# Kernel tuning notes

Hardware: AMD Instinct MI355X
Metric: run time of the kernel (lower is better)

Reference implementation:

```python
import jax, jax.numpy as jnp
import numpy as np

B, T, D = 16, 2048, 64


def setup_inputs() -> dict:
    key = jax.random.key(0)
    kq, kk, kv, kb = jax.random.split(key, 4)
    q = jax.random.normal(kq, (B, T, D), dtype=jnp.float32)
    k = jax.random.normal(kk, (B, T, D), dtype=jnp.float32)
    v = jax.random.normal(kv, (B, T, D), dtype=jnp.float32)
    add_attn = jax.random.normal(kb, (B, T, T), dtype=jnp.float32)
    return {"q": q, "k": k, "v": v, "add_attn": add_attn}


def reference(q, k, v, add_attn):
    # scale = 1/sqrt(head_dim), the standard value passed by callers
    scale = 1.0 / jnp.sqrt(jnp.asarray(q.shape[-1], dtype=q.dtype))
    # [B, T, T] attention logits: bmm(q, k^T) * scale + additive bias
    attn = jnp.einsum('btd,bsd->bts', q, k) * scale + add_attn
    # softmax over keys (dim=2); dropout p=0.0 is identity
    attn = jax.nn.softmax(attn, axis=2)
    # [B, T, D] weighted values
    output = jnp.einsum('bts,bsd->btd', attn, v)
    return (output, attn)
```

## Files before the change

kernel.cpp:

```cpp
#include <hip/hip_runtime.h>
#include <stdint.h>

#define NB 16
#define NT 2048
#define ND 64

typedef __attribute__((ext_vector_type(8))) short bf16x8;
typedef __attribute__((ext_vector_type(4))) float f32x4;
typedef __attribute__((ext_vector_type(4))) _Float16 f16x4;

__device__ __forceinline__ unsigned short f2bf(float f) {
    union { float f; unsigned u; } v; v.f = f;
    unsigned r = v.u + 0x7fffu + ((v.u >> 16) & 1u);
    return (unsigned short)(r >> 16);
}
__device__ __forceinline__ unsigned short f2h(float f) {
    union { _Float16 h; unsigned short u; } v; v.h = (_Float16)f; return v.u;
}

__global__ __launch_bounds__(256) void prep_k(const float* __restrict__ Q,
                                              const float* __restrict__ K,
                                              const float* __restrict__ V,
                                              unsigned short* __restrict__ qbf,
                                              unsigned short* __restrict__ kbf,
                                              unsigned short* __restrict__ vt)
{
    const size_t i = (size_t)blockIdx.x * 256 + threadIdx.x;
    const int which = blockIdx.y;
    if (which == 2) {
        float4 v4 = ((const float4*)V)[i];
        const int d4 = (int)(i & 15);
        const int t  = (int)((i >> 4) & (NT - 1));
        const int b  = (int)(i >> 15);
        unsigned short* base = vt + ((size_t)b * ND + d4 * 4) * NT + t;
        base[0]      = f2h(v4.x);
        base[NT]     = f2h(v4.y);
        base[2 * NT] = f2h(v4.z);
        base[3 * NT] = f2h(v4.w);
    } else {
        const float4* src = (which == 0) ? (const float4*)Q : (const float4*)K;
        unsigned short* dst = (which == 0) ? qbf : kbf;
        float4 v4 = src[i];
        union { unsigned short s[4]; unsigned long long ll; } u;
        u.s[0] = f2bf(v4.x); u.s[1] = f2bf(v4.y);
        u.s[2] = f2bf(v4.z); u.s[3] = f2bf(v4.w);
        *(unsigned long long*)(dst + 4 * i) = u.ll;
    }
}

__global__ __launch_bounds__(512, 4)
void attn_onepass(const unsigned short* __restrict__ qbf,
                  const unsigned short* __restrict__ kbf,
                  const unsigned short* __restrict__ vt,
                  const float* __restrict__ Bias,
                  float* __restrict__ Out,
                  float* __restrict__ Attn)
{
    const int flat = blockIdx.x + (NT / 16) * blockIdx.y;
    const int lin  = (flat & 7) * 256 + (flat >> 3);
    const int b    = lin >> 7;
    const int q0   = (lin & 127) * 16;

    const int tid = threadIdx.x, w = tid >> 6, lane = tid & 63;
    const int n = lane & 15, qd = lane >> 4;
    const int kw0 = w * 256;

    __shared__ float s_rs[8][16];
    __shared__ float s_o[8 * 16 * 68];

    const unsigned short* qp = qbf + ((size_t)(b * NT + q0 + n)) * ND + qd * 8;
    const bf16x8 qf0 = *(const bf16x8*)qp;
    const bf16x8 qf1 = *(const bf16x8*)(qp + 32);
    const float* Bb = Bias + ((size_t)b * NT + q0 + n) * NT;
    float* Ab = Attn + ((size_t)b * NT + q0 + n) * NT;
    const unsigned short* vtb = vt + (size_t)b * ND * NT + (size_t)n * NT;
    const unsigned short* kbp = kbf + ((size_t)(b * NT + kw0 + n)) * ND + qd * 8;
    const float* bbp = Bb + kw0 + qd * 4;

    f16x4 ev[16];
    bf16x8 kb0[2], kb1[2];
    float4 bb[4];
#pragma unroll
    for (int i = 0; i < 2; ++i) {
        const unsigned short* kp = kbp + (size_t)(16 * i) * ND;
        kb0[i] = *(const bf16x8*)kp;
        kb1[i] = *(const bf16x8*)(kp + 32);
    }
#pragma unroll
    for (int i = 0; i < 4; ++i)
        bb[i] = *(const float4*)(bbp + 16 * i);
    __builtin_amdgcn_sched_barrier(0);

    float rs = 0.f;
#pragma unroll
    for (int t = 0; t < 16; ++t) {
        const bf16x8 kf0 = kb0[t & 1];
        const bf16x8 kf1 = kb1[t & 1];
        const float4 bs = bb[t & 3];
        f32x4 acc = {0.f, 0.f, 0.f, 0.f};
        acc = __builtin_amdgcn_mfma_f32_16x16x32_bf16(kf0, qf0, acc, 0, 0, 0);
        acc = __builtin_amdgcn_mfma_f32_16x16x32_bf16(kf1, qf1, acc, 0, 0, 0);
        float e0 = __expf(__builtin_fmaf(acc[0], 0.125f, bs.x - 2.0f));
        float e1 = __expf(__builtin_fmaf(acc[1], 0.125f, bs.y - 2.0f));
        float e2 = __expf(__builtin_fmaf(acc[2], 0.125f, bs.z - 2.0f));
        float e3 = __expf(__builtin_fmaf(acc[3], 0.125f, bs.w - 2.0f));
        union { _Float16 h[4]; f16x4 v; } u;
        u.h[0] = (_Float16)e0; u.h[1] = (_Float16)e1;
        u.h[2] = (_Float16)e2; u.h[3] = (_Float16)e3;
        ev[t] = u.v;
        rs += (e0 + e1) + (e2 + e3);
        __builtin_amdgcn_sched_barrier(0);
        if (t + 2 < 16) {
            const unsigned short* kp = kbp + (size_t)(16 * (t + 2)) * ND;
            kb0[t & 1] = *(const bf16x8*)kp;
            kb1[t & 1] = *(const bf16x8*)(kp + 32);
        }
        if (t + 4 < 16)
            bb[t & 3] = *(const float4*)(bbp + 16 * (t + 4));
        __builtin_amdgcn_sched_barrier(0);
    }

    f16x4 vr0[2][4], vr1[2][4];
#pragma unroll
    for (int i = 0; i < 2; ++i)
#pragma unroll
        for (int dt = 0; dt < 4; ++dt) {
            const unsigned short* vp = vtb + kw0 + 32 * i + qd * 4 + (size_t)dt * 16 * NT;
            vr0[i][dt] = *(const f16x4*)(const void*)vp;
            vr1[i][dt] = *(const f16x4*)(const void*)(vp + 16);
        }
    __builtin_amdgcn_sched_barrier(0);

    rs += __shfl_xor(rs, 16, 64);
    rs += __shfl_xor(rs, 32, 64);
    if (lane < 16) s_rs[w][lane] = rs;
    __syncthreads();
    const float tot = ((s_rs[0][n] + s_rs[1][n]) + (s_rs[2][n] + s_rs[3][n])) +
                      ((s_rs[4][n] + s_rs[5][n]) + (s_rs[6][n] + s_rs[7][n]));
    const float inv = 1.0f / tot;

    f32x4 oacc[4];
#pragma unroll
    for (int dt = 0; dt < 4; ++dt) oacc[dt] = (f32x4){0.f, 0.f, 0.f, 0.f};

#pragma unroll
    for (int tp = 0; tp < 8; ++tp) {
        const int key0 = kw0 + 32 * tp;
        const f16x4 e0v = ev[2 * tp];
        const f16x4 e1v = ev[2 * tp + 1];
        float4 s0, s1;
        s0.x = (float)e0v[0] * inv; s0.y = (float)e0v[1] * inv;
        s0.z = (float)e0v[2] * inv; s0.w = (float)e0v[3] * inv;
        s1.x = (float)e1v[0] * inv; s1.y = (float)e1v[1] * inv;
        s1.z = (float)e1v[2] * inv; s1.w = (float)e1v[3] * inv;
        *(float4*)(Ab + key0 + qd * 4) = s0;
        *(float4*)(Ab + key0 + 16 + qd * 4) = s1;
#pragma unroll
        for (int dt = 0; dt < 4; ++dt) {
            oacc[dt] = __builtin_amdgcn_mfma_f32_16x16x16f16(vr0[tp & 1][dt], e0v, oacc[dt], 0, 0, 0);
            oacc[dt] = __builtin_amdgcn_mfma_f32_16x16x16f16(vr1[tp & 1][dt], e1v, oacc[dt], 0, 0, 0);
        }
        __builtin_amdgcn_sched_barrier(0);
        if (tp + 2 < 8) {
#pragma unroll
            for (int dt = 0; dt < 4; ++dt) {
                const unsigned short* vp =
                    vtb + kw0 + 32 * (tp + 2) + qd * 4 + (size_t)dt * 16 * NT;
                vr0[tp & 1][dt] = *(const f16x4*)(const void*)vp;
                vr1[tp & 1][dt] = *(const f16x4*)(const void*)(vp + 16);
            }
        }
        __builtin_amdgcn_sched_barrier(0);
    }

#pragma unroll
    for (int dt = 0; dt < 4; ++dt) {
        float4 t4;
        t4.x = oacc[dt][0] * inv; t4.y = oacc[dt][1] * inv;
        t4.z = oacc[dt][2] * inv; t4.w = oacc[dt][3] * inv;
        *(float4*)&s_o[(w * 16 + n) * 68 + dt * 16 + qd * 4] = t4;
    }
    __syncthreads();
    if (tid < 256) {
        const int row = tid >> 4, d4 = (tid & 15) * 4;
        float4 o0 = *(const float4*)&s_o[(0 * 16 + row) * 68 + d4];
        float4 o1 = *(const float4*)&s_o[(1 * 16 + row) * 68 + d4];
        float4 o2 = *(const float4*)&s_o[(2 * 16 + row) * 68 + d4];
        float4 o3 = *(const float4*)&s_o[(3 * 16 + row) * 68 + d4];
        float4 o4 = *(const float4*)&s_o[(4 * 16 + row) * 68 + d4];
        float4 o5 = *(const float4*)&s_o[(5 * 16 + row) * 68 + d4];
        float4 o6 = *(const float4*)&s_o[(6 * 16 + row) * 68 + d4];
        float4 o7 = *(const float4*)&s_o[(7 * 16 + row) * 68 + d4];
        float4 o;
        o.x = ((o0.x + o1.x) + (o2.x + o3.x)) + ((o4.x + o5.x) + (o6.x + o7.x));
        o.y = ((o0.y + o1.y) + (o2.y + o3.y)) + ((o4.y + o5.y) + (o6.y + o7.y));
        o.z = ((o0.z + o1.z) + (o2.z + o3.z)) + ((o4.z + o5.z) + (o6.z + o7.z));
        o.w = ((o0.w + o1.w) + (o2.w + o3.w)) + ((o4.w + o5.w) + (o6.w + o7.w));
        *(float4*)(Out + ((size_t)b * NT + q0 + row) * ND + d4) = o;
    }
}

__device__ __forceinline__ bf16x8 pack8(float4 a, float4 b) {
    union { unsigned short s[8]; bf16x8 v; } u;
    u.s[0] = f2bf(a.x); u.s[1] = f2bf(a.y); u.s[2] = f2bf(a.z); u.s[3] = f2bf(a.w);
    u.s[4] = f2bf(b.x); u.s[5] = f2bf(b.y); u.s[6] = f2bf(b.z); u.s[7] = f2bf(b.w);
    return u.v;
}
__global__ __launch_bounds__(256, 2)
void attn_fused(const float* __restrict__ Q, const float* __restrict__ K,
                const float* __restrict__ V, const float* __restrict__ Bias,
                float* __restrict__ Out, float* __restrict__ Attn)
{
    const int b  = blockIdx.y;
    const int q0 = blockIdx.x * 16;
    const int tid  = threadIdx.x;
    const int w    = tid >> 6;
    const int lane = tid & 63;
    const int n  = lane & 15;
    const int qd = lane >> 4;
    const int kw0 = w * 512;
    __shared__ float s_rs[4][16];
    __shared__ __align__(16) unsigned char s_rp[4][16 * 80];
    const float* Qb = Q + ((size_t)b * NT + q0) * ND;
    const float* Kb = K + (size_t)b * NT * ND;
    const float* Vb = V + (size_t)b * NT * ND;
    const float* Bb = Bias + ((size_t)b * NT + q0) * NT;
    float* Ab = Attn + ((size_t)b * NT + q0) * NT;
    float* Ob = Out  + ((size_t)b * NT + q0) * ND;
    bf16x8 qf0, qf1;
    {
        const float* qp = Qb + n * ND + qd * 8;
        qf0 = pack8(*(const float4*)qp,        *(const float4*)(qp + 4));
        qf1 = pack8(*(const float4*)(qp + 32), *(const float4*)(qp + 36));
    }
    float ev[32][4];
    float rs = 0.f;
#pragma unroll
    for (int t = 0; t < 32; ++t) {
        const int key0 = kw0 + 16 * t;
        const float* kp = Kb + (size_t)(key0 + n) * ND + qd * 8;
        bf16x8 kf0 = pack8(*(const float4*)kp,        *(const float4*)(kp + 4));
        bf16x8 kf1 = pack8(*(const float4*)(kp + 32), *(const float4*)(kp + 36));
        f32x4 acc = {0.f, 0.f, 0.f, 0.f};
        acc = __builtin_amdgcn_mfma_f32_16x16x32_bf16(kf0, qf0, acc, 0, 0, 0);
        acc = __builtin_amdgcn_mfma_f32_16x16x32_bf16(kf1, qf1, acc, 0, 0, 0);
        float4 bs = *(const float4*)(Bb + (size_t)n * NT + key0 + qd * 4);
        float e0 = __expf(acc[0] * 0.125f + bs.x);
        float e1 = __expf(acc[1] * 0.125f + bs.y);
        float e2 = __expf(acc[2] * 0.125f + bs.z);
        float e3 = __expf(acc[3] * 0.125f + bs.w);
        ev[t][0] = e0; ev[t][1] = e1; ev[t][2] = e2; ev[t][3] = e3;
        rs += (e0 + e1) + (e2 + e3);
    }
    rs += __shfl_xor(rs, 16, 64);
    rs += __shfl_xor(rs, 32, 64);
    if (lane < 16) s_rs[w][lane] = rs;
    __syncthreads();
    const float tot = (s_rs[0][n] + s_rs[1][n]) + (s_rs[2][n] + s_rs[3][n]);
    const float inv = 1.0f / tot;
    f32x4 oacc[4];
#pragma unroll
    for (int dt = 0; dt < 4; ++dt) oacc[dt] = (f32x4){0.f, 0.f, 0.f, 0.f};
    unsigned char* rp = &s_rp[w][0];
#pragma unroll
    for (int c = 0; c < 16; ++c) {
        const int kbase = kw0 + 32 * c;
#pragma unroll
        for (int tt = 0; tt < 2; ++tt) {
            const int t = 2 * c + tt;
            float p0 = ev[t][0] * inv;
            float p1 = ev[t][1] * inv;
            float p2 = ev[t][2] * inv;
            float p3 = ev[t][3] * inv;
            float4 pv; pv.x = p0; pv.y = p1; pv.z = p2; pv.w = p3;
            *(float4*)(Ab + (size_t)n * NT + kbase + 16 * tt + qd * 4) = pv;
            union { unsigned short s[4]; unsigned long long ll; } pu;
            pu.s[0] = f2bf(p0); pu.s[1] = f2bf(p1);
            pu.s[2] = f2bf(p2); pu.s[3] = f2bf(p3);
            *(unsigned long long*)(rp + n * 80 + (16 * tt + 4 * qd) * 2) = pu.ll;
        }
        __syncthreads();
        bf16x8 pf;
        {
            union { uint4 u; bf16x8 v; } uu;
            uu.u = *(const uint4*)(rp + n * 80 + qd * 16);
            pf = uu.v;
        }
#pragma unroll
        for (int dt = 0; dt < 4; ++dt) {
            const int d = dt * 16 + n;
            const float* vp = Vb + (size_t)(kbase + qd * 8) * ND + d;
            float4 va, vb4;
            va.x  = vp[0];   va.y  = vp[64];  va.z  = vp[128]; va.w  = vp[192];
            vb4.x = vp[256]; vb4.y = vp[320]; vb4.z = vp[384]; vb4.w = vp[448];
            bf16x8 vf = pack8(va, vb4);
            oacc[dt] = __builtin_amdgcn_mfma_f32_16x16x32_bf16(vf, pf, oacc[dt], 0, 0, 0);
        }
        __syncthreads();
    }
#pragma unroll
    for (int dt = 0; dt < 4; ++dt)
#pragma unroll
        for (int r = 0; r < 4; ++r)
            atomicAdd(Ob + (size_t)n * ND + dt * 16 + qd * 4 + r, oacc[dt][r]);
}

extern "C" void kernel_launch(void* const* d_in, const int* in_sizes, int n_in,
                              void* d_out, int out_size, void* d_ws, size_t ws_size,
                              hipStream_t stream)
{
    const float* q    = (const float*)d_in[0];
    const float* k    = (const float*)d_in[1];
    const float* v    = (const float*)d_in[2];
    const float* bias = (const float*)d_in[3];
    float* out  = (float*)d_out;
    float* attn = out + (size_t)NB * NT * ND;

    const size_t elems = (size_t)NB * NT * ND;
    const size_t need  = 3 * elems * 2;

    if (ws_size >= need) {
        unsigned short* qbf = (unsigned short*)d_ws;
        unsigned short* kbf = qbf + elems;
        unsigned short* vtb = kbf + elems;
        prep_k<<<dim3((unsigned)(elems / 4 / 256), 3), 256, 0, stream>>>(q, k, v, qbf, kbf, vtb);
        attn_onepass<<<dim3(NT / 16, NB), 512, 0, stream>>>(qbf, kbf, vtb, bias, out, attn);
    } else {
        hipMemsetAsync(out, 0, (size_t)NB * NT * ND * sizeof(float), stream);
        dim3 grid(NT / 16, NB);
        attn_fused<<<grid, 256, 0, stream>>>(q, k, v, bias, out, attn);
    }
}
```

Measured before the change: 252.2 us.

## Stage attention probabilities in LDS for coalesced full-row nontemporal stores

Unnormalized fp16 probabilities are written to a 64 KB swizzled LDS staging buffer instead of being stored straight to global memory in scattered 16-byte pieces per lane. After a barrier, each thread normalizes and writes contiguous row segments of the attention matrix with nontemporal stores. The goal is better coalescing and less cache pollution for the large attn output write. The cost is much higher LDS use, so occupancy drops from 4 to 2 blocks, and there is an extra barrier plus an LDS round trip.

```diff
diff --git a/kernel.cpp b/kernel.cpp
--- a/kernel.cpp
+++ b/kernel.cpp
@@ -48,7 +48,7 @@
     }
 }
 
-__global__ __launch_bounds__(512, 4)
+__global__ __launch_bounds__(512, 2)
 void attn_onepass(const unsigned short* __restrict__ qbf,
                   const unsigned short* __restrict__ kbf,
                   const unsigned short* __restrict__ vt,
@@ -65,14 +65,14 @@
     const int n = lane & 15, qd = lane >> 4;
     const int kw0 = w * 256;
 
+    __shared__ __align__(16) unsigned char stg_[16 * 4096];
     __shared__ float s_rs[8][16];
-    __shared__ float s_o[8 * 16 * 68];
+    __shared__ float s_inv[16];
 
     const unsigned short* qp = qbf + ((size_t)(b * NT + q0 + n)) * ND + qd * 8;
     const bf16x8 qf0 = *(const bf16x8*)qp;
     const bf16x8 qf1 = *(const bf16x8*)(qp + 32);
     const float* Bb = Bias + ((size_t)b * NT + q0 + n) * NT;
-    float* Ab = Attn + ((size_t)b * NT + q0 + n) * NT;
     const unsigned short* vtb = vt + (size_t)b * ND * NT + (size_t)n * NT;
     const unsigned short* kbp = kbf + ((size_t)(b * NT + kw0 + n)) * ND + qd * 8;
     const float* bbp = Bb + kw0 + qd * 4;
@@ -138,6 +138,7 @@
     const float tot = ((s_rs[0][n] + s_rs[1][n]) + (s_rs[2][n] + s_rs[3][n])) +
                       ((s_rs[4][n] + s_rs[5][n]) + (s_rs[6][n] + s_rs[7][n]));
     const float inv = 1.0f / tot;
+    if (tid < 16) s_inv[tid] = inv;
 
     f32x4 oacc[4];
 #pragma unroll
@@ -145,16 +146,15 @@
 
 #pragma unroll
     for (int tp = 0; tp < 8; ++tp) {
-        const int key0 = kw0 + 32 * tp;
         const f16x4 e0v = ev[2 * tp];
         const f16x4 e1v = ev[2 * tp + 1];
-        float4 s0, s1;
-        s0.x = (float)e0v[0] * inv; s0.y = (float)e0v[1] * inv;
-        s0.z = (float)e0v[2] * inv; s0.w = (float)e0v[3] * inv;
-        s1.x = (float)e1v[0] * inv; s1.y = (float)e1v[1] * inv;
-        s1.z = (float)e1v[2] * inv; s1.w = (float)e1v[3] * inv;
-        *(float4*)(Ab + key0 + qd * 4) = s0;
-        *(float4*)(Ab + key0 + 16 + qd * 4) = s1;
+        {
+            const int ow0 = (kw0 + 32 * tp + qd * 4) * 2;
+            const int c = (n & 7) << 4;
+            char* rowb = (char*)stg_ + n * 4096;
+            *(f16x4*)(rowb + (ow0 ^ c)) = e0v;
+            *(f16x4*)(rowb + ((ow0 + 32) ^ c)) = e1v;
+        }
 #pragma unroll
         for (int dt = 0; dt < 4; ++dt) {
             oacc[dt] = __builtin_amdgcn_mfma_f32_16x16x16f16(vr0[tp & 1][dt], e0v, oacc[dt], 0, 0, 0);
@@ -173,6 +173,21 @@
         __builtin_amdgcn_sched_barrier(0);
     }
 
+    __syncthreads();
+#pragma unroll
+    for (int r = 0; r < 16; ++r) {
+        const int orw = (tid * 8) ^ ((r & 7) << 4);
+        const f16x4 hv = *(const f16x4*)(stg_ + r * 4096 + orw);
+        const float sinv = s_inv[r];
+        f32x4 o4;
+        o4[0] = (float)hv[0] * sinv; o4[1] = (float)hv[1] * sinv;
+        o4[2] = (float)hv[2] * sinv; o4[3] = (float)hv[3] * sinv;
+        __builtin_nontemporal_store(
+            o4, (f32x4*)(Attn + ((size_t)(b * NT + q0 + r)) * NT + tid * 4));
+    }
+
+    __syncthreads();
+    float* s_o = (float*)stg_;
 #pragma unroll
     for (int dt = 0; dt < 4; ++dt) {
         float4 t4;
```

After: 255.8 us. No clear change (+1.4%).

## Deepen score-phase prefetch with async bias-to-LDS ring and explicit vmcnt waits

Applied to the files above, without the earlier changes.

The bias tiles now stream into a per-wave six-slot LDS ring via global_load_lds, and K fragments are loaded six steps ahead with inline-asm global loads. Hand-counted s_waitcnt vmcnt values replace compiler-managed waits, so more memory traffic is in flight during the QK^T/exp loop. The output-reduction scratch reuses the same LDS pool after a barrier. In exchange it uses more registers and LDS and lowers launch-bounds occupancy from 4 to 2 blocks per CU. It also depends on exact vmcnt accounting, which is fragile if the compiler inserts other loads.

```diff
diff --git a/kernel.cpp b/kernel.cpp
--- a/kernel.cpp
+++ b/kernel.cpp
@@ -16,6 +16,20 @@
 }
 __device__ __forceinline__ unsigned short f2h(float f) {
     union { _Float16 h; unsigned short u; } v; v.h = (_Float16)f; return v.u;
+}
+
+template <int N>
+__device__ __forceinline__ void waitvm() {
+    asm volatile("s_waitcnt vmcnt(%0)" ::"n"(N) : "memory");
+    __builtin_amdgcn_sched_barrier(0);
+}
+__device__ __forceinline__ void ld_b128(bf16x8& d, const unsigned short* p) {
+    asm volatile("global_load_dwordx4 %0, %1, off" : "=v"(d) : "v"(p) : "memory");
+}
+typedef __attribute__((address_space(1))) const unsigned int gas_u32;
+typedef __attribute__((address_space(3))) unsigned int las_u32;
+__device__ __forceinline__ void async16(const void* g, void* l) {
+    __builtin_amdgcn_global_load_lds((gas_u32*)g, (las_u32*)l, 16, 0, 0);
 }
 
 __global__ __launch_bounds__(256) void prep_k(const float* __restrict__ Q,
@@ -48,7 +62,7 @@
     }
 }
 
-__global__ __launch_bounds__(512, 4)
+__global__ __launch_bounds__(512, 2)
 void attn_onepass(const unsigned short* __restrict__ qbf,
                   const unsigned short* __restrict__ kbf,
                   const unsigned short* __restrict__ vt,
@@ -65,38 +79,46 @@
     const int n = lane & 15, qd = lane >> 4;
     const int kw0 = w * 256;
 
+    __shared__ float pool[12288];
     __shared__ float s_rs[8][16];
-    __shared__ float s_o[8 * 16 * 68];
-
-    const unsigned short* qp = qbf + ((size_t)(b * NT + q0 + n)) * ND + qd * 8;
-    const bf16x8 qf0 = *(const bf16x8*)qp;
-    const bf16x8 qf1 = *(const bf16x8*)(qp + 32);
+
     const float* Bb = Bias + ((size_t)b * NT + q0 + n) * NT;
     float* Ab = Attn + ((size_t)b * NT + q0 + n) * NT;
     const unsigned short* vtb = vt + (size_t)b * ND * NT + (size_t)n * NT;
     const unsigned short* kbp = kbf + ((size_t)(b * NT + kw0 + n)) * ND + qd * 8;
-    const float* bbp = Bb + kw0 + qd * 4;
+    const float* bsrc = Bb + kw0 + qd * 4;
+    float* ringb = &pool[(w * 6) * 256];
+
+    bf16x8 qf0, qf1;
+    {
+        const unsigned short* qp = qbf + ((size_t)(b * NT + q0 + n)) * ND + qd * 8;
+        ld_b128(qf0, qp);
+        ld_b128(qf1, qp + 32);
+    }
 
     f16x4 ev[16];
-    bf16x8 kb0[2], kb1[2];
-    float4 bb[4];
-#pragma unroll
-    for (int i = 0; i < 2; ++i) {
-        const unsigned short* kp = kbp + (size_t)(16 * i) * ND;
-        kb0[i] = *(const bf16x8*)kp;
-        kb1[i] = *(const bf16x8*)(kp + 32);
-    }
-#pragma unroll
-    for (int i = 0; i < 4; ++i)
-        bb[i] = *(const float4*)(bbp + 16 * i);
+    bf16x8 kb0[6], kb1[6];
+
+#pragma unroll
+    for (int i = 0; i < 6; ++i) {
+        async16(bsrc + 16 * i, ringb + i * 256);
+        ld_b128(kb0[i], kbp + (size_t)(16 * i) * ND);
+        ld_b128(kb1[i], kbp + (size_t)(16 * i) * ND + 32);
+    }
     __builtin_amdgcn_sched_barrier(0);
 
     float rs = 0.f;
 #pragma unroll
     for (int t = 0; t < 16; ++t) {
-        const bf16x8 kf0 = kb0[t & 1];
-        const bf16x8 kf1 = kb1[t & 1];
-        const float4 bs = bb[t & 3];
+        if      (t <= 10) waitvm<15>();
+        else if (t == 11) waitvm<12>();
+        else if (t == 12) waitvm<9>();
+        else if (t == 13) waitvm<6>();
+        else if (t == 14) waitvm<3>();
+        else              waitvm<0>();
+        const float4 bs = *(const float4*)(ringb + (t % 6) * 256 + lane * 4);
+        const bf16x8 kf0 = kb0[t % 6];
+        const bf16x8 kf1 = kb1[t % 6];
         f32x4 acc = {0.f, 0.f, 0.f, 0.f};
         acc = __builtin_amdgcn_mfma_f32_16x16x32_bf16(kf0, qf0, acc, 0, 0, 0);
         acc = __builtin_amdgcn_mfma_f32_16x16x32_bf16(kf1, qf1, acc, 0, 0, 0);
@@ -110,13 +132,11 @@
         ev[t] = u.v;
         rs += (e0 + e1) + (e2 + e3);
         __builtin_amdgcn_sched_barrier(0);
-        if (t + 2 < 16) {
-            const unsigned short* kp = kbp + (size_t)(16 * (t + 2)) * ND;
-            kb0[t & 1] = *(const bf16x8*)kp;
-            kb1[t & 1] = *(const bf16x8*)(kp + 32);
-        }
-        if (t + 4 < 16)
-            bb[t & 3] = *(const float4*)(bbp + 16 * (t + 4));
+        if (t + 6 < 16) {
+            async16(bsrc + 16 * (t + 6), ringb + (t % 6) * 256);
+            ld_b128(kb0[t % 6], kbp + (size_t)(16 * (t + 6)) * ND);
+            ld_b128(kb1[t % 6], kbp + (size_t)(16 * (t + 6)) * ND + 32);
+        }
         __builtin_amdgcn_sched_barrier(0);
     }
 
@@ -173,6 +193,8 @@
         __builtin_amdgcn_sched_barrier(0);
     }
 
+    __syncthreads();
+    float* s_o = pool;
 #pragma unroll
     for (int dt = 0; dt < 4; ++dt) {
         float4 t4;
```

Result: no change. 257.0 us (+1.9%).
